# Performance work log

Measured on AMD Instinct MI355X. Metric: run time of the kernel, lower is better.

Reference implementation:

```python
import jax, jax.numpy as jnp
import numpy as np

N_NODES = 100000
N_EDGES = 50000
NNZ = 1600000
C_IN = 128
C_OUT = 128
BN_EPS = 1e-5


def setup_inputs() -> dict:
    key = jax.random.key(0)
    k_x, k_ni, k_ei, k_w, k_W, k_b = jax.random.split(key, 6)
    x = jax.random.normal(k_x, (N_NODES, C_IN), dtype=jnp.float32)
    node_idx = jax.random.randint(k_ni, (NNZ,), 0, N_NODES, dtype=jnp.int64)
    edge_idx = jax.random.randint(k_ei, (NNZ,), 0, N_EDGES, dtype=jnp.int64)
    hyperedge_index = jnp.stack([node_idx, edge_idx], axis=0)  # [2, nnz]
    hyperedge_weight = jax.random.uniform(k_w, (N_EDGES,), dtype=jnp.float32)
    W = jax.random.normal(k_W, (C_IN, C_OUT), dtype=jnp.float32) * (1.0 / np.sqrt(C_IN))
    b = jax.random.normal(k_b, (C_OUT,), dtype=jnp.float32) * 0.02
    gamma = jnp.ones((C_OUT,), dtype=jnp.float32)
    beta = jnp.zeros((C_OUT,), dtype=jnp.float32)
    return {"x": x, "hyperedge_index": hyperedge_index,
            "hyperedge_weight": hyperedge_weight, "W": W, "b": b,
            "gamma": gamma, "beta": beta}


def reference(x, hyperedge_index, hyperedge_weight, W, b, gamma, beta):
    # HypergraphConv (PyG semantics): out = D^{-1} H B^{-1} H^T (X W) + b
    # D_v = sum_{e: v in e} w_e  (hyperedge weights enter via node degree),
    # B_e = |e| (number of incident nodes).
    N = x.shape[0]
    E = hyperedge_weight.shape[0]
    node_idx = hyperedge_index[0]
    edge_idx = hyperedge_index[1]

    xt = x @ W  # [N, C_out]

    # Node degree D (weighted) and hyperedge degree B.
    D = jax.ops.segment_sum(hyperedge_weight[edge_idx], node_idx, num_segments=N)
    D_inv = jnp.where(D > 0, 1.0 / D, 0.0)  # inf -> 0
    Bdeg = jax.ops.segment_sum(jnp.ones(edge_idx.shape, dtype=xt.dtype),
                               edge_idx, num_segments=E)
    B_inv = jnp.where(Bdeg > 0, 1.0 / Bdeg, 0.0)

    # node -> hyperedge aggregation: e = B^{-1} sum_{v in e} xt_v
    e_feat = jax.ops.segment_sum(xt[node_idx], edge_idx, num_segments=E)
    e_feat = e_feat * B_inv[:, None]  # [E, C_out]

    # hyperedge -> node aggregation: out_v = D^{-1} sum_{e ni v} e_feat_e
    out = jax.ops.segment_sum(e_feat[edge_idx], node_idx, num_segments=N)
    out = out * D_inv[:, None] + b  # [N, C_out]

    # BatchNorm (training-mode batch statistics over nodes)
    mean = jnp.mean(out, axis=0)
    var = jnp.mean(jnp.square(out - mean), axis=0)  # biased, as BatchNorm1d
    out = (out - mean) * jax.lax.rsqrt(var + BN_EPS) * gamma + beta

    # SiLU activation
    out = out * jax.nn.sigmoid(out)
    # NOTE: original code computes `x = out + x` for the skip but returns `out`,
    # so the skip is a no-op; we faithfully return `out` (use_skip=False here).
    return out
```

## Files before the change

### kernel.cpp

```cpp
#include <hip/hip_runtime.h>
#include <cstdint>
#include <cstddef>

#define CC 128
#define LOG_FINE 7
#define FINE 128
#define CAPE 6144
#define CAPV 3072
#define BIN_TILE 4096

typedef __attribute__((ext_vector_type(8))) short bf16x8;
typedef __attribute__((ext_vector_type(4))) float f32x4;

__device__ __forceinline__ unsigned f2b(float f) {
    const unsigned u = __float_as_uint(f);
    return (u + 0x7fffu + ((u >> 16) & 1u)) >> 16;
}
__device__ __forceinline__ float b2f_lo(unsigned u) { return __uint_as_float(u << 16); }
__device__ __forceinline__ float b2f_hi(unsigned u) { return __uint_as_float(u & 0xffff0000u); }

__global__ __launch_bounds__(512) void prep(const int* __restrict__ nidx,
                                            const int* __restrict__ eidx,
                                            int* __restrict__ curE,
                                            int* __restrict__ curV,
                                            unsigned* __restrict__ binnedE,
                                            unsigned* __restrict__ binnedV,
                                            int nnz, int nbE, int nbV, int nbin,
                                            const float4* __restrict__ xin,
                                            uint2* __restrict__ xh, int n4) {
    __shared__ int cntE[512], gposE[512];
    __shared__ int cntV[1024], gposV[1024];
    const int tid = threadIdx.x;
    if (blockIdx.x >= (unsigned)nbin) {
        const int bid = blockIdx.x - nbin;
        const int nblk = gridDim.x - nbin;
        for (int i = bid * 512 + tid; i < n4; i += nblk * 512) {
            const float4 v = xin[i];
            xh[i] = make_uint2(f2b(v.x) | (f2b(v.y) << 16), f2b(v.z) | (f2b(v.w) << 16));
        }
        return;
    }
    for (int i = tid; i < nbE; i += 512) cntE[i] = 0;
    for (int i = tid; i < nbV; i += 512) cntV[i] = 0;
    __syncthreads();
    const int base = blockIdx.x * BIN_TILE;
    int pE[8], rE[8], pV[8], rV[8];
#pragma unroll
    for (int j = 0; j < 8; ++j) {
        const int i = base + tid + j * 512;
        if (i < nnz) {
            const int e = eidx[i], v = nidx[i];
            const int bE = e >> LOG_FINE, bV = v >> LOG_FINE;
            rE[j] = (bE << 16) | atomicAdd(&cntE[bE], 1);
            pE[j] = (v << LOG_FINE) | (e & (FINE - 1));
            rV[j] = (bV << 16) | atomicAdd(&cntV[bV], 1);
            pV[j] = (e << LOG_FINE) | (v & (FINE - 1));
        } else { rE[j] = -1; rV[j] = -1; }
    }
    __syncthreads();
    for (int i = tid; i < nbE; i += 512) {
        const int c = cntE[i];
        gposE[i] = (c > 0) ? atomicAdd(&curE[i], c) : 0;
    }
    for (int i = tid; i < nbV; i += 512) {
        const int c = cntV[i];
        gposV[i] = (c > 0) ? atomicAdd(&curV[i], c) : 0;
    }
    __syncthreads();
#pragma unroll
    for (int j = 0; j < 8; ++j) {
        if (rE[j] >= 0) {
            const int b = rE[j] >> 16;
            binnedE[(size_t)b * CAPE + gposE[b] + (rE[j] & 0xffff)] = (unsigned)pE[j];
        }
        if (rV[j] >= 0) {
            const int b = rV[j] >> 16;
            binnedV[(size_t)b * CAPV + gposV[b] + (rV[j] & 0xffff)] = (unsigned)pV[j];
        }
    }
}

__global__ __launch_bounds__(256) void bfrag_prep(const float* __restrict__ W,
                                                  uint4* __restrict__ Bfrag) {
    const int idx = blockIdx.x * 256 + threadIdx.x;
    if (idx >= 2048) return;
    const int lane = idx & 63, t = idx >> 6;
    const int kk = t >> 3, nt = t & 7;
    const int k0 = kk * 32 + (lane >> 4) * 8;
    const int n = nt * 16 + (lane & 15);
    unsigned r[4];
#pragma unroll
    for (int p = 0; p < 4; ++p) {
        const float w0 = W[(size_t)(k0 + 2 * p) * CC + n];
        const float w1 = W[(size_t)(k0 + 2 * p + 1) * CC + n];
        r[p] = f2b(w0) | (f2b(w1) << 16);
    }
    Bfrag[idx] = make_uint4(r[0], r[1], r[2], r[3]);
}

__global__ __launch_bounds__(512) void fill_all(const int* __restrict__ curE,
                                                const int* __restrict__ curV,
                                                unsigned* __restrict__ binnedE,
                                                unsigned* __restrict__ binnedV,
                                                const float* __restrict__ hw,
                                                int2* __restrict__ rowsE,
                                                int2* __restrict__ rowsV,
                                                float* __restrict__ Dinv,
                                                int E, int N, int nbE) {
    __shared__ unsigned vals[CAPE];
    __shared__ int scnt[FINE], soff[FINE], sscan[FINE];
    __shared__ float sd[FINE];
    const int tid = threadIdx.x;
    const bool isE = (blockIdx.x < (unsigned)nbE);
    const int b = isE ? blockIdx.x : blockIdx.x - nbE;
    const int cap = isE ? CAPE : CAPV;
    const int base = b * cap;
    const int cnt = isE ? curE[b] : curV[b];
    unsigned* binned = isE ? binnedE : binnedV;
    int2* rows = isE ? rowsE : rowsV;
    const int nrows = isE ? E : N;
    for (int i = tid; i < cnt; i += 512) vals[i] = binned[base + i];
    if (tid < FINE) { scnt[tid] = 0; sd[tid] = 0.f; }
    __syncthreads();
    for (int i = tid; i < cnt; i += 512) atomicAdd(&scnt[vals[i] & (FINE - 1)], 1);
    __syncthreads();
    if (tid < FINE) sscan[tid] = scnt[tid];
    __syncthreads();
#pragma unroll
    for (int d = 1; d < FINE; d <<= 1) {
        int t = 0;
        if (tid >= d && tid < FINE) t = sscan[tid - d];
        __syncthreads();
        if (tid < FINE) sscan[tid] += t;
        __syncthreads();
    }
    if (tid < FINE) {
        const int excl = sscan[tid] - scnt[tid];
        soff[tid] = excl;
        const int row = (b << LOG_FINE) + tid;
        if (row < nrows) rows[row] = make_int2(base + excl, base + excl + scnt[tid]);
    }
    __syncthreads();
    if (isE) {
        for (int i = tid; i < cnt; i += 512) {
            const unsigned p = vals[i];
            const int slot = (int)(p & (FINE - 1));
            const int pos = base + atomicAdd(&soff[slot], 1);
            binned[pos] = p >> LOG_FINE;
        }
    } else {
        for (int i = tid; i < cnt; i += 512) {
            const unsigned p = vals[i];
            const int slot = (int)(p & (FINE - 1));
            const int e = (int)(p >> LOG_FINE);
            const int pos = base + atomicAdd(&soff[slot], 1);
            binned[pos] = (unsigned)e;
            atomicAdd(&sd[slot], hw[e]);
        }
        __syncthreads();
        if (tid < FINE) {
            const int row = (b << LOG_FINE) + tid;
            if (row < N) {
                const float d = sd[tid];
                Dinv[row] = (d > 0.f) ? 1.f / d : 0.f;
            }
        }
    }
}

__global__ __launch_bounds__(512) void n2e_mm(const int2* __restrict__ rowsE,
                                              const unsigned* __restrict__ binnedE,
                                              const uint4* __restrict__ xh4,
                                              const uint4* __restrict__ Bfrag,
                                              unsigned short* __restrict__ efeat, int E) {
    __shared__ uint4 tile[16][17];
    const int tid = threadIdx.x;
    const int sub = tid >> 5;
    const int half = (tid >> 4) & 1;
    const int q = tid & 15;
    const int e = blockIdx.x * 16 + sub;
    float a[8];
#pragma unroll
    for (int k = 0; k < 8; ++k) a[k] = 0.f;
    int s = 0, t = 0;
    if (e < E) {
        const int2 st = rowsE[e];
        s = st.x; t = st.y;
        int j = s;
        for (; j + 7 < t; j += 8) {
            const int v0 = (int)binnedE[j + 0 + half];
            const int v1 = (int)binnedE[j + 2 + half];
            const int v2 = (int)binnedE[j + 4 + half];
            const int v3 = (int)binnedE[j + 6 + half];
            const uint4 u0 = xh4[(size_t)v0 * 16 + q];
            const uint4 u1 = xh4[(size_t)v1 * 16 + q];
            const uint4 u2 = xh4[(size_t)v2 * 16 + q];
            const uint4 u3 = xh4[(size_t)v3 * 16 + q];
            a[0] += b2f_lo(u0.x) + b2f_lo(u1.x) + b2f_lo(u2.x) + b2f_lo(u3.x);
            a[1] += b2f_hi(u0.x) + b2f_hi(u1.x) + b2f_hi(u2.x) + b2f_hi(u3.x);
            a[2] += b2f_lo(u0.y) + b2f_lo(u1.y) + b2f_lo(u2.y) + b2f_lo(u3.y);
            a[3] += b2f_hi(u0.y) + b2f_hi(u1.y) + b2f_hi(u2.y) + b2f_hi(u3.y);
            a[4] += b2f_lo(u0.z) + b2f_lo(u1.z) + b2f_lo(u2.z) + b2f_lo(u3.z);
            a[5] += b2f_hi(u0.z) + b2f_hi(u1.z) + b2f_hi(u2.z) + b2f_hi(u3.z);
            a[6] += b2f_lo(u0.w) + b2f_lo(u1.w) + b2f_lo(u2.w) + b2f_lo(u3.w);
            a[7] += b2f_hi(u0.w) + b2f_hi(u1.w) + b2f_hi(u2.w) + b2f_hi(u3.w);
        }
        for (; j + 1 < t; j += 2) {
            const int v0 = (int)binnedE[j + half];
            const uint4 u = xh4[(size_t)v0 * 16 + q];
            a[0] += b2f_lo(u.x); a[1] += b2f_hi(u.x);
            a[2] += b2f_lo(u.y); a[3] += b2f_hi(u.y);
            a[4] += b2f_lo(u.z); a[5] += b2f_hi(u.z);
            a[6] += b2f_lo(u.w); a[7] += b2f_hi(u.w);
        }
        if (j < t && half == 0) {
            const uint4 u = xh4[(size_t)binnedE[j] * 16 + q];
            a[0] += b2f_lo(u.x); a[1] += b2f_hi(u.x);
            a[2] += b2f_lo(u.y); a[3] += b2f_hi(u.y);
            a[4] += b2f_lo(u.z); a[5] += b2f_hi(u.z);
            a[6] += b2f_lo(u.w); a[7] += b2f_hi(u.w);
        }
    }
#pragma unroll
    for (int k = 0; k < 8; ++k) a[k] += __shfl_xor(a[k], 16);
    if (half == 0) {
        const float binv = (t > s) ? 1.f / (float)(t - s) : 0.f;
#pragma unroll
        for (int k = 0; k < 8; ++k) a[k] *= binv;
        uint4 o;
        o.x = f2b(a[0]) | (f2b(a[1]) << 16);
        o.y = f2b(a[2]) | (f2b(a[3]) << 16);
        o.z = f2b(a[4]) | (f2b(a[5]) << 16);
        o.w = f2b(a[6]) | (f2b(a[7]) << 16);
        tile[sub][q] = o;
    }
    __syncthreads();
    const int w = tid >> 6;
    const int lane = tid & 63;
    const int g = lane >> 4;
    const int c = lane & 15;
    uint4 af[4];
#pragma unroll
    for (int kk = 0; kk < 4; ++kk) af[kk] = tile[lane & 15][kk * 4 + g];
    f32x4 acc = (f32x4){0.f, 0.f, 0.f, 0.f};
#pragma unroll
    for (int kk = 0; kk < 4; ++kk) {
        const uint4 bv = Bfrag[(kk * 8 + w) * 64 + lane];
        acc = __builtin_amdgcn_mfma_f32_16x16x32_bf16(
            *(const bf16x8*)&af[kk], *(const bf16x8*)&bv, acc, 0, 0, 0);
    }
#pragma unroll
    for (int r = 0; r < 4; ++r) {
        const int row = blockIdx.x * 16 + g * 4 + r;
        if (row < E) efeat[(size_t)row * CC + w * 16 + c] = (unsigned short)f2b(acc[r]);
    }
}

__global__ __launch_bounds__(256) void gather_e2n_bn(const int2* __restrict__ rows,
                                                     const unsigned* __restrict__ lst,
                                                     const uint4* __restrict__ ef4,
                                                     const float* __restrict__ Dinv,
                                                     const float* __restrict__ b,
                                                     uint4* __restrict__ oh,
                                                     float* __restrict__ copies, int N) {
    __shared__ float bl[8][256];
    const int tid = threadIdx.x;
    for (int i = tid; i < 2048; i += 256) ((float*)bl)[i] = 0.f;
    __syncthreads();
    const int sub = tid >> 5;
    const int half = (tid >> 4) & 1;
    const int q = tid & 15;
    const int v = blockIdx.x * 8 + sub;
    if (v < N) {
        const int2 st = rows[v];
        const int s = st.x, t = st.y;
        float a[8];
#pragma unroll
        for (int k = 0; k < 8; ++k) a[k] = 0.f;
        int j = s;
        for (; j + 7 < t; j += 8) {
            const int e0 = (int)lst[j + 0 + half];
            const int e1 = (int)lst[j + 2 + half];
            const int e2 = (int)lst[j + 4 + half];
            const int e3 = (int)lst[j + 6 + half];
            const uint4 u0 = ef4[(size_t)e0 * 16 + q];
            const uint4 u1 = ef4[(size_t)e1 * 16 + q];
            const uint4 u2 = ef4[(size_t)e2 * 16 + q];
            const uint4 u3 = ef4[(size_t)e3 * 16 + q];
            a[0] += b2f_lo(u0.x) + b2f_lo(u1.x) + b2f_lo(u2.x) + b2f_lo(u3.x);
            a[1] += b2f_hi(u0.x) + b2f_hi(u1.x) + b2f_hi(u2.x) + b2f_hi(u3.x);
            a[2] += b2f_lo(u0.y) + b2f_lo(u1.y) + b2f_lo(u2.y) + b2f_lo(u3.y);
            a[3] += b2f_hi(u0.y) + b2f_hi(u1.y) + b2f_hi(u2.y) + b2f_hi(u3.y);
            a[4] += b2f_lo(u0.z) + b2f_lo(u1.z) + b2f_lo(u2.z) + b2f_lo(u3.z);
            a[5] += b2f_hi(u0.z) + b2f_hi(u1.z) + b2f_hi(u2.z) + b2f_hi(u3.z);
            a[6] += b2f_lo(u0.w) + b2f_lo(u1.w) + b2f_lo(u2.w) + b2f_lo(u3.w);
            a[7] += b2f_hi(u0.w) + b2f_hi(u1.w) + b2f_hi(u2.w) + b2f_hi(u3.w);
        }
        for (; j + 1 < t; j += 2) {
            const int e0 = (int)lst[j + half];
            const uint4 u = ef4[(size_t)e0 * 16 + q];
            a[0] += b2f_lo(u.x); a[1] += b2f_hi(u.x);
            a[2] += b2f_lo(u.y); a[3] += b2f_hi(u.y);
            a[4] += b2f_lo(u.z); a[5] += b2f_hi(u.z);
            a[6] += b2f_lo(u.w); a[7] += b2f_hi(u.w);
        }
        if (j < t && half == 0) {
            const uint4 u = ef4[(size_t)lst[j] * 16 + q];
            a[0] += b2f_lo(u.x); a[1] += b2f_hi(u.x);
            a[2] += b2f_lo(u.y); a[3] += b2f_hi(u.y);
            a[4] += b2f_lo(u.z); a[5] += b2f_hi(u.z);
            a[6] += b2f_lo(u.w); a[7] += b2f_hi(u.w);
        }
#pragma unroll
        for (int k = 0; k < 8; ++k) a[k] += __shfl_xor(a[k], 16);
        if (half == 0) {
            const float dinv = Dinv[v];
            const float4 b0 = *(const float4*)&b[8 * q];
            const float4 b1 = *(const float4*)&b[8 * q + 4];
            float o[8];
            o[0] = a[0] * dinv + b0.x; o[1] = a[1] * dinv + b0.y;
            o[2] = a[2] * dinv + b0.z; o[3] = a[3] * dinv + b0.w;
            o[4] = a[4] * dinv + b1.x; o[5] = a[5] * dinv + b1.y;
            o[6] = a[6] * dinv + b1.z; o[7] = a[7] * dinv + b1.w;
            uint4 ov;
            ov.x = f2b(o[0]) | (f2b(o[1]) << 16);
            ov.y = f2b(o[2]) | (f2b(o[3]) << 16);
            ov.z = f2b(o[4]) | (f2b(o[5]) << 16);
            ov.w = f2b(o[6]) | (f2b(o[7]) << 16);
            oh[(size_t)v * 16 + q] = ov;
            *(float4*)&bl[sub][8 * q]       = make_float4(o[0], o[1], o[2], o[3]);
            *(float4*)&bl[sub][8 * q + 4]   = make_float4(o[4], o[5], o[6], o[7]);
            *(float4*)&bl[sub][128 + 8 * q] = make_float4(o[0] * o[0], o[1] * o[1],
                                                          o[2] * o[2], o[3] * o[3]);
            *(float4*)&bl[sub][132 + 8 * q] = make_float4(o[4] * o[4], o[5] * o[5],
                                                          o[6] * o[6], o[7] * o[7]);
        }
    }
    __syncthreads();
    float s = 0.f;
#pragma unroll
    for (int i = 0; i < 8; ++i) s += bl[i][tid];
    atomicAdd(&copies[(blockIdx.x & 63) * 256 + tid], s);
}

__global__ __launch_bounds__(256) void bn_silu(const uint2* __restrict__ oh2,
                                               const float* __restrict__ copies,
                                               const float* __restrict__ gamma,
                                               const float* __restrict__ beta,
                                               float* __restrict__ out, int N) {
    __shared__ float sl[256];
    const int tid = threadIdx.x;
    float s = 0.f;
#pragma unroll 8
    for (int i = 0; i < 64; ++i) s += copies[i * 256 + tid];
    sl[tid] = s;
    __syncthreads();
    const int sub = tid >> 5;
    const int lane = tid & 31;
    const int c4 = lane * 4;
    const float invN = 1.0f / (float)N;
    float g[4], bb[4];
#pragma unroll
    for (int k = 0; k < 4; ++k) {
        const float mean = sl[c4 + k] * invN;
        float var = sl[128 + c4 + k] * invN - mean * mean;
        var = fmaxf(var, 0.f);
        const float istd = rsqrtf(var + 1e-5f);
        g[k] = gamma[c4 + k] * istd;
        bb[k] = beta[c4 + k] - mean * g[k];
    }
    for (int v = blockIdx.x * 8 + sub; v < N; v += gridDim.x * 8) {
        const uint2 u = oh2[(size_t)v * 32 + lane];
        float y[4];
        y[0] = b2f_lo(u.x); y[1] = b2f_hi(u.x);
        y[2] = b2f_lo(u.y); y[3] = b2f_hi(u.y);
        float4 o;
#pragma unroll
        for (int k = 0; k < 4; ++k) {
            const float z = y[k] * g[k] + bb[k];
            (&o.x)[k] = z / (1.f + __expf(-z));
        }
        *(float4*)&out[(size_t)v * CC + c4] = o;
    }
}

extern "C" void kernel_launch(void* const* d_in, const int* in_sizes, int n_in,
                              void* d_out, int out_size, void* d_ws, size_t ws_size,
                              hipStream_t stream) {
    const float* x     = (const float*)d_in[0];
    const int*   hidx  = (const int*)d_in[1];
    const float* hw    = (const float*)d_in[2];
    const float* W     = (const float*)d_in[3];
    const float* b     = (const float*)d_in[4];
    const float* gamma = (const float*)d_in[5];
    const float* beta  = (const float*)d_in[6];

    const int N   = in_sizes[0] / CC;
    const int nnz = in_sizes[1] / 2;
    const int E   = in_sizes[2];

    const int* nidx = hidx;
    const int* eidx = hidx + nnz;

    float* out = (float*)d_out;

    const int nbE = (E + FINE - 1) / FINE;
    const int nbV = (N + FINE - 1) / FINE;

    unsigned* ws      = (unsigned*)d_ws;
    unsigned* xh      = ws;
    unsigned* efeat   = xh + (size_t)N * 64;
    int2*     rowsE   = (int2*)(efeat + (size_t)E * 64);
    int2*     rowsV   = rowsE + E;
    float*    Dinv    = (float*)(rowsV + N);
    float*    copies  = Dinv + N;
    int*      curE    = (int*)(copies + 64 * 256);
    int*      curV    = curE + nbE;
    unsigned* binnedE = (unsigned*)(curV + nbV);
    unsigned* binnedV = binnedE + (size_t)nbE * CAPE;
    uintptr_t bfaddr  = (uintptr_t)(binnedV + (size_t)nbV * CAPV);
    uint4*    Bfrag   = (uint4*)((bfaddr + 15) & ~(uintptr_t)15);

    hipMemsetAsync(copies, 0, (64 * 256 + (size_t)nbE + nbV) * sizeof(int), stream);

    const int nbin = (nnz + BIN_TILE - 1) / BIN_TILE;
    const int ncvt = 256;
    prep<<<nbin + ncvt, 512, 0, stream>>>(nidx, eidx, curE, curV, binnedE, binnedV,
                                          nnz, nbE, nbV, nbin,
                                          (const float4*)x, (uint2*)xh, N * CC / 4);
    bfrag_prep<<<8, 256, 0, stream>>>(W, Bfrag);

    fill_all<<<nbE + nbV, 512, 0, stream>>>(curE, curV, binnedE, binnedV, hw,
                                            rowsE, rowsV, Dinv, E, N, nbE);

    n2e_mm<<<(E + 15) / 16, 512, 0, stream>>>(rowsE, binnedE, (const uint4*)xh,
                                              Bfrag, (unsigned short*)efeat, E);

    gather_e2n_bn<<<(N + 7) / 8, 256, 0, stream>>>(rowsV, binnedV, (const uint4*)efeat,
                                                   Dinv, b, (uint4*)xh, copies, N);

    bn_silu<<<1024, 256, 0, stream>>>((const uint2*)xh, copies, gamma, beta, out, N);
}
```

Measured before the change: 220.6 us.

## Split fused node-to-edge gather+matmul into separate gather and MFMA kernels

Folds the Bfrag weight-conversion kernel into the prep kernel as extra blocks, which saves one launch. It also splits the fused n2e_mm kernel into two. gather_n2e uses 256-thread blocks and writes raw bf16 edge sums to a new workspace buffer, and mm_mfma has each wave compute a 16x128 output tile with MFMA. This decouples the gather's occupancy from the matmul's shared-memory tile and barrier, at the cost of an extra E x 128 bf16 round trip through global memory and one more launch.

Result: slower. 227.0 us (+2.9%).

```diff
diff --git a/kernel.cpp b/kernel.cpp
--- a/kernel.cpp
+++ b/kernel.cpp
@@ -25,16 +25,35 @@
                                             int* __restrict__ curV,
                                             unsigned* __restrict__ binnedE,
                                             unsigned* __restrict__ binnedV,
-                                            int nnz, int nbE, int nbV, int nbin,
+                                            int nnz, int nbE, int nbV, int nbin, int ncvt,
                                             const float4* __restrict__ xin,
-                                            uint2* __restrict__ xh, int n4) {
+                                            uint2* __restrict__ xh, int n4,
+                                            const float* __restrict__ W,
+                                            uint4* __restrict__ Bfrag) {
     __shared__ int cntE[512], gposE[512];
     __shared__ int cntV[1024], gposV[1024];
     const int tid = threadIdx.x;
+    if (blockIdx.x >= (unsigned)(nbin + ncvt)) {
+        const int idx = (blockIdx.x - nbin - ncvt) * 512 + tid;
+        if (idx < 2048) {
+            const int lane = idx & 63, t = idx >> 6;
+            const int kk = t >> 3, nt = t & 7;
+            const int k0 = kk * 32 + (lane >> 4) * 8;
+            const int n = nt * 16 + (lane & 15);
+            unsigned r[4];
+#pragma unroll
+            for (int p = 0; p < 4; ++p) {
+                const float w0 = W[(size_t)(k0 + 2 * p) * CC + n];
+                const float w1 = W[(size_t)(k0 + 2 * p + 1) * CC + n];
+                r[p] = f2b(w0) | (f2b(w1) << 16);
+            }
+            Bfrag[idx] = make_uint4(r[0], r[1], r[2], r[3]);
+        }
+        return;
+    }
     if (blockIdx.x >= (unsigned)nbin) {
         const int bid = blockIdx.x - nbin;
-        const int nblk = gridDim.x - nbin;
-        for (int i = bid * 512 + tid; i < n4; i += nblk * 512) {
+        for (int i = bid * 512 + tid; i < n4; i += ncvt * 512) {
             const float4 v = xin[i];
             xh[i] = make_uint2(f2b(v.x) | (f2b(v.y) << 16), f2b(v.z) | (f2b(v.w) << 16));
         }
@@ -78,24 +97,6 @@
             binnedV[(size_t)b * CAPV + gposV[b] + (rV[j] & 0xffff)] = (unsigned)pV[j];
         }
     }
-}
-
-__global__ __launch_bounds__(256) void bfrag_prep(const float* __restrict__ W,
-                                                  uint4* __restrict__ Bfrag) {
-    const int idx = blockIdx.x * 256 + threadIdx.x;
-    if (idx >= 2048) return;
-    const int lane = idx & 63, t = idx >> 6;
-    const int kk = t >> 3, nt = t & 7;
-    const int k0 = kk * 32 + (lane >> 4) * 8;
-    const int n = nt * 16 + (lane & 15);
-    unsigned r[4];
-#pragma unroll
-    for (int p = 0; p < 4; ++p) {
-        const float w0 = W[(size_t)(k0 + 2 * p) * CC + n];
-        const float w1 = W[(size_t)(k0 + 2 * p + 1) * CC + n];
-        r[p] = f2b(w0) | (f2b(w1) << 16);
-    }
-    Bfrag[idx] = make_uint4(r[0], r[1], r[2], r[3]);
 }
 
 __global__ __launch_bounds__(512) void fill_all(const int* __restrict__ curE,
@@ -168,58 +169,53 @@
     }
 }
 
-__global__ __launch_bounds__(512) void n2e_mm(const int2* __restrict__ rowsE,
-                                              const unsigned* __restrict__ binnedE,
-                                              const uint4* __restrict__ xh4,
-                                              const uint4* __restrict__ Bfrag,
-                                              unsigned short* __restrict__ efeat, int E) {
-    __shared__ uint4 tile[16][17];
-    const int tid = threadIdx.x;
-    const int sub = tid >> 5;
-    const int half = (tid >> 4) & 1;
-    const int q = tid & 15;
-    const int e = blockIdx.x * 16 + sub;
+__global__ __launch_bounds__(256) void gather_n2e(const int2* __restrict__ rows,
+                                                  const unsigned* __restrict__ lst,
+                                                  const uint4* __restrict__ xh4,
+                                                  uint4* __restrict__ eraw4, int E) {
+    const int sub = threadIdx.x >> 5;
+    const int half = (threadIdx.x >> 4) & 1;
+    const int q = threadIdx.x & 15;
+    const int e = blockIdx.x * 8 + sub;
+    if (e >= E) return;
+    const int2 st = rows[e];
+    const int s = st.x, t = st.y;
     float a[8];
 #pragma unroll
     for (int k = 0; k < 8; ++k) a[k] = 0.f;
-    int s = 0, t = 0;
-    if (e < E) {
-        const int2 st = rowsE[e];
-        s = st.x; t = st.y;
-        int j = s;
-        for (; j + 7 < t; j += 8) {
-            const int v0 = (int)binnedE[j + 0 + half];
-            const int v1 = (int)binnedE[j + 2 + half];
-            const int v2 = (int)binnedE[j + 4 + half];
-            const int v3 = (int)binnedE[j + 6 + half];
-            const uint4 u0 = xh4[(size_t)v0 * 16 + q];
-            const uint4 u1 = xh4[(size_t)v1 * 16 + q];
-            const uint4 u2 = xh4[(size_t)v2 * 16 + q];
-            const uint4 u3 = xh4[(size_t)v3 * 16 + q];
-            a[0] += b2f_lo(u0.x) + b2f_lo(u1.x) + b2f_lo(u2.x) + b2f_lo(u3.x);
-            a[1] += b2f_hi(u0.x) + b2f_hi(u1.x) + b2f_hi(u2.x) + b2f_hi(u3.x);
-            a[2] += b2f_lo(u0.y) + b2f_lo(u1.y) + b2f_lo(u2.y) + b2f_lo(u3.y);
-            a[3] += b2f_hi(u0.y) + b2f_hi(u1.y) + b2f_hi(u2.y) + b2f_hi(u3.y);
-            a[4] += b2f_lo(u0.z) + b2f_lo(u1.z) + b2f_lo(u2.z) + b2f_lo(u3.z);
-            a[5] += b2f_hi(u0.z) + b2f_hi(u1.z) + b2f_hi(u2.z) + b2f_hi(u3.z);
-            a[6] += b2f_lo(u0.w) + b2f_lo(u1.w) + b2f_lo(u2.w) + b2f_lo(u3.w);
-            a[7] += b2f_hi(u0.w) + b2f_hi(u1.w) + b2f_hi(u2.w) + b2f_hi(u3.w);
-        }
-        for (; j + 1 < t; j += 2) {
-            const int v0 = (int)binnedE[j + half];
-            const uint4 u = xh4[(size_t)v0 * 16 + q];
-            a[0] += b2f_lo(u.x); a[1] += b2f_hi(u.x);
-            a[2] += b2f_lo(u.y); a[3] += b2f_hi(u.y);
-            a[4] += b2f_lo(u.z); a[5] += b2f_hi(u.z);
-            a[6] += b2f_lo(u.w); a[7] += b2f_hi(u.w);
-        }
-        if (j < t && half == 0) {
-            const uint4 u = xh4[(size_t)binnedE[j] * 16 + q];
-            a[0] += b2f_lo(u.x); a[1] += b2f_hi(u.x);
-            a[2] += b2f_lo(u.y); a[3] += b2f_hi(u.y);
-            a[4] += b2f_lo(u.z); a[5] += b2f_hi(u.z);
-            a[6] += b2f_lo(u.w); a[7] += b2f_hi(u.w);
-        }
+    int j = s;
+    for (; j + 7 < t; j += 8) {
+        const int v0 = (int)lst[j + 0 + half];
+        const int v1 = (int)lst[j + 2 + half];
+        const int v2 = (int)lst[j + 4 + half];
+        const int v3 = (int)lst[j + 6 + half];
+        const uint4 u0 = xh4[(size_t)v0 * 16 + q];
+        const uint4 u1 = xh4[(size_t)v1 * 16 + q];
+        const uint4 u2 = xh4[(size_t)v2 * 16 + q];
+        const uint4 u3 = xh4[(size_t)v3 * 16 + q];
+        a[0] += b2f_lo(u0.x) + b2f_lo(u1.x) + b2f_lo(u2.x) + b2f_lo(u3.x);
+        a[1] += b2f_hi(u0.x) + b2f_hi(u1.x) + b2f_hi(u2.x) + b2f_hi(u3.x);
+        a[2] += b2f_lo(u0.y) + b2f_lo(u1.y) + b2f_lo(u2.y) + b2f_lo(u3.y);
+        a[3] += b2f_hi(u0.y) + b2f_hi(u1.y) + b2f_hi(u2.y) + b2f_hi(u3.y);
+        a[4] += b2f_lo(u0.z) + b2f_lo(u1.z) + b2f_lo(u2.z) + b2f_lo(u3.z);
+        a[5] += b2f_hi(u0.z) + b2f_hi(u1.z) + b2f_hi(u2.z) + b2f_hi(u3.z);
+        a[6] += b2f_lo(u0.w) + b2f_lo(u1.w) + b2f_lo(u2.w) + b2f_lo(u3.w);
+        a[7] += b2f_hi(u0.w) + b2f_hi(u1.w) + b2f_hi(u2.w) + b2f_hi(u3.w);
+    }
+    for (; j + 1 < t; j += 2) {
+        const int v0 = (int)lst[j + half];
+        const uint4 u = xh4[(size_t)v0 * 16 + q];
+        a[0] += b2f_lo(u.x); a[1] += b2f_hi(u.x);
+        a[2] += b2f_lo(u.y); a[3] += b2f_hi(u.y);
+        a[4] += b2f_lo(u.z); a[5] += b2f_hi(u.z);
+        a[6] += b2f_lo(u.w); a[7] += b2f_hi(u.w);
+    }
+    if (j < t && half == 0) {
+        const uint4 u = xh4[(size_t)lst[j] * 16 + q];
+        a[0] += b2f_lo(u.x); a[1] += b2f_hi(u.x);
+        a[2] += b2f_lo(u.y); a[3] += b2f_hi(u.y);
+        a[4] += b2f_lo(u.z); a[5] += b2f_hi(u.z);
+        a[6] += b2f_lo(u.w); a[7] += b2f_hi(u.w);
     }
 #pragma unroll
     for (int k = 0; k < 8; ++k) a[k] += __shfl_xor(a[k], 16);
@@ -232,27 +228,44 @@
         o.y = f2b(a[2]) | (f2b(a[3]) << 16);
         o.z = f2b(a[4]) | (f2b(a[5]) << 16);
         o.w = f2b(a[6]) | (f2b(a[7]) << 16);
-        tile[sub][q] = o;
-    }
-    __syncthreads();
-    const int w = tid >> 6;
-    const int lane = tid & 63;
+        eraw4[(size_t)e * 16 + q] = o;
+    }
+}
+
+__global__ __launch_bounds__(256) void mm_mfma(const uint4* __restrict__ A4,
+                                               const uint4* __restrict__ Bfrag,
+                                               unsigned short* __restrict__ Out, int M) {
+    const int lane = threadIdx.x & 63;
+    const int wave = threadIdx.x >> 6;
+    const int row0 = blockIdx.x * 64 + wave * 16;
     const int g = lane >> 4;
     const int c = lane & 15;
-    uint4 af[4];
-#pragma unroll
-    for (int kk = 0; kk < 4; ++kk) af[kk] = tile[lane & 15][kk * 4 + g];
-    f32x4 acc = (f32x4){0.f, 0.f, 0.f, 0.f};
+    const int arow = row0 + c;
+    uint4 a[4];
 #pragma unroll
     for (int kk = 0; kk < 4; ++kk) {
-        const uint4 bv = Bfrag[(kk * 8 + w) * 64 + lane];
-        acc = __builtin_amdgcn_mfma_f32_16x16x32_bf16(
-            *(const bf16x8*)&af[kk], *(const bf16x8*)&bv, acc, 0, 0, 0);
-    }
-#pragma unroll
-    for (int r = 0; r < 4; ++r) {
-        const int row = blockIdx.x * 16 + g * 4 + r;
-        if (row < E) efeat[(size_t)row * CC + w * 16 + c] = (unsigned short)f2b(acc[r]);
+        a[kk] = (arow < M) ? A4[(size_t)arow * 16 + kk * 4 + g]
+                           : make_uint4(0u, 0u, 0u, 0u);
+    }
+    f32x4 acc[8];
+#pragma unroll
+    for (int nt = 0; nt < 8; ++nt) acc[nt] = (f32x4){0.f, 0.f, 0.f, 0.f};
+#pragma unroll
+    for (int nt = 0; nt < 8; ++nt) {
+#pragma unroll
+        for (int kk = 0; kk < 4; ++kk) {
+            const uint4 bv = Bfrag[(kk * 8 + nt) * 64 + lane];
+            acc[nt] = __builtin_amdgcn_mfma_f32_16x16x32_bf16(
+                *(const bf16x8*)&a[kk], *(const bf16x8*)&bv, acc[nt], 0, 0, 0);
+        }
+    }
+#pragma unroll
+    for (int nt = 0; nt < 8; ++nt) {
+#pragma unroll
+        for (int r = 0; r < 4; ++r) {
+            const int row = row0 + g * 4 + r;
+            if (row < M) Out[(size_t)row * CC + nt * 16 + c] = (unsigned short)f2b(acc[nt][r]);
+        }
     }
 }
 
@@ -409,7 +422,8 @@
 
     unsigned* ws      = (unsigned*)d_ws;
     unsigned* xh      = ws;
-    unsigned* efeat   = xh + (size_t)N * 64;
+    unsigned* eraw    = xh + (size_t)N * 64;
+    unsigned* efeat   = eraw + (size_t)E * 64;
     int2*     rowsE   = (int2*)(efeat + (size_t)E * 64);
     int2*     rowsV   = rowsE + E;
     float*    Dinv    = (float*)(rowsV + N);
@@ -425,16 +439,19 @@
 
     const int nbin = (nnz + BIN_TILE - 1) / BIN_TILE;
     const int ncvt = 256;
-    prep<<<nbin + ncvt, 512, 0, stream>>>(nidx, eidx, curE, curV, binnedE, binnedV,
-                                          nnz, nbE, nbV, nbin,
-                                          (const float4*)x, (uint2*)xh, N * CC / 4);
-    bfrag_prep<<<8, 256, 0, stream>>>(W, Bfrag);
+    prep<<<nbin + ncvt + 4, 512, 0, stream>>>(nidx, eidx, curE, curV, binnedE, binnedV,
+                                              nnz, nbE, nbV, nbin, ncvt,
+                                              (const float4*)x, (uint2*)xh, N * CC / 4,
+                                              W, Bfrag);
 
     fill_all<<<nbE + nbV, 512, 0, stream>>>(curE, curV, binnedE, binnedV, hw,
                                             rowsE, rowsV, Dinv, E, N, nbE);
 
-    n2e_mm<<<(E + 15) / 16, 512, 0, stream>>>(rowsE, binnedE, (const uint4*)xh,
-                                              Bfrag, (unsigned short*)efeat, E);
+    gather_n2e<<<(E + 7) / 8, 256, 0, stream>>>(rowsE, binnedE, (const uint4*)xh,
+                                                (uint4*)eraw, E);
+
+    mm_mfma<<<(E + 63) / 64, 256, 0, stream>>>((const uint4*)eraw, Bfrag,
+                                               (unsigned short*)efeat, E);
 
     gather_e2n_bn<<<(N + 7) / 8, 256, 0, stream>>>(rowsV, binnedV, (const uint4*)efeat,
                                                    Dinv, b, (uint4*)xh, copies, N);
```
